# Performance work log

Measured on AMD Instinct MI355X. Metric: run time of the kernel, lower is better.

Reference implementation:

```python
import jax, jax.numpy as jnp
import numpy as np

B, T, H = 512, 512, 256
IN = 2


def setup_inputs() -> dict:
    key = jax.random.key(0)
    k1, k2, k3, k4, k5, k6 = jax.random.split(key, 6)
    inputs = jax.random.normal(k1, (B, T, IN), dtype=jnp.float32)
    # lengths in [1, T] so outputs[v-1] is always valid
    input_len = jax.random.randint(k2, (B,), 1, T + 1, dtype=jnp.int64)
    h0 = jnp.zeros((B, H), dtype=jnp.float32)
    s = 1.0 / np.sqrt(H)
    W_ih = jax.random.uniform(k3, (3 * H, IN), jnp.float32, -s, s)
    W_hh = jax.random.uniform(k4, (3 * H, H), jnp.float32, -s, s)
    b_ih = jax.random.uniform(k5, (3 * H,), jnp.float32, -s, s)
    b_hh = jax.random.uniform(k6, (3 * H,), jnp.float32, -s, s)
    return {"inputs": inputs, "input_len": input_len, "h0": h0,
            "W_ih": W_ih, "W_hh": W_hh, "b_ih": b_ih, "b_hh": b_hh}


def _gru_scan(inputs, h0, W_ih, W_hh, b_ih, b_hh):
    # Precompute input projections for all timesteps: [T, B, 3H]
    gi_all = jnp.einsum('bti,gi->tbg', inputs, W_ih) + b_ih

    def step(h, gi):
        gh = h @ W_hh.T + b_hh                      # [B, 3H]
        gi_r, gi_z, gi_n = jnp.split(gi, 3, axis=-1)
        gh_r, gh_z, gh_n = jnp.split(gh, 3, axis=-1)
        r = jax.nn.sigmoid(gi_r + gh_r)
        z = jax.nn.sigmoid(gi_z + gh_z)
        n = jnp.tanh(gi_n + r * gh_n)
        h_new = (1.0 - z) * n + z * h
        return h_new, h_new

    _, hs = jax.lax.scan(step, h0, gi_all)          # hs: [T, B, H]
    return hs


def reference(inputs, input_len, h0, W_ih, W_hh, b_ih, b_hh):
    hs = _gru_scan(inputs, h0, W_ih, W_hh, b_ih, b_hh)   # [T, B, H]
    # per-batch gather of hidden state at timestep (len - 1)
    b_idx = jnp.arange(inputs.shape[0])
    return hs[input_len - 1, b_idx]                      # [B, H]
```

## Files before the change

kernel.cpp:

```cpp
#include <hip/hip_runtime.h>
#include <stdint.h>


typedef int   v4i   __attribute__((ext_vector_type(4)));
typedef float f32x4 __attribute__((ext_vector_type(4)));

#define BB 512
#define TT 512
#define HH 256
#define NCT 48
#define KTI 4
#define HSTR8 320
#define WSCALE 2032.0f
#define INVS (1.0f/(2032.0f*127.0f))

__global__ void prep_pack_i8(const float* __restrict__ Whh, uint4* __restrict__ Wp) {
    int n = blockIdx.x * blockDim.x + threadIdx.x;
    int lane = n & 63;
    int kt = (n >> 6) & (KTI - 1);
    int ct = n >> 8;
    int row = 16 * ct + (lane & 15);
    int k0  = 64 * kt + (lane >> 4) * 16;
    const float* src = Whh + (size_t)row * HH + k0;
    uint dw[4];
    #pragma unroll
    for (int d = 0; d < 4; ++d) {
        uint acc = 0;
        #pragma unroll
        for (int j = 0; j < 4; ++j) {
            int q = (int)rintf(src[4 * d + j] * WSCALE);
            q = q < -127 ? -127 : (q > 127 ? 127 : q);
            acc |= ((uint)(q & 0xff)) << (8 * j);
        }
        dw[d] = acc;
    }
    Wp[n] = uint4{dw[0], dw[1], dw[2], dw[3]};
}

__device__ __forceinline__ float sigmoid_f(float x) {
    return __builtin_amdgcn_rcpf(1.f + __expf(-x));
}
__device__ __forceinline__ float tanh_f(float x) {
    x = fminf(fmaxf(x, -15.f), 15.f);
    float e = __expf(-2.f * x);
    return (1.f - e) * __builtin_amdgcn_rcpf(1.f + e);
}

__global__ void __launch_bounds__(512, 1)
gru_persist(const float* __restrict__ x,
            const int* __restrict__ len,
            const float* __restrict__ h0,
            const float* __restrict__ Wih,
            const float* __restrict__ bih,
            const float* __restrict__ bhh,
            const uint4* __restrict__ Wp,
            float* __restrict__ out)
{
    __shared__ __align__(16) int8_t h8[2][2][HSTR8];

    const int tid  = threadIdx.x;
    const int lane = tid & 63;
    const int w    = tid >> 6;
    const int b0   = blockIdx.x * 2;

    v4i wfr[6][KTI];
    {
        const int cts[6] = {2*w, 2*w+1, 16+2*w, 16+2*w+1, 32+2*w, 32+2*w+1};
        #pragma unroll
        for (int c = 0; c < 6; ++c)
            #pragma unroll
            for (int kt = 0; kt < KTI; ++kt)
                wfr[c][kt] = __builtin_bit_cast(v4i, Wp[(cts[c] * KTI + kt) * 64 + lane]);
    }
    #pragma unroll
    for (int c = 0; c < 6; ++c)
        #pragma unroll
        for (int kt = 0; kt < KTI; ++kt)
            asm volatile("" : "+v"(wfr[c][kt]));

    const int batch = (lane >> 4) & 1;
    const int e = 32 * w + (lane & 15) + ((lane >> 5) << 4);

    const float ccx = bih[e] + bhh[e];
    const float ccy = bih[HH + e] + bhh[HH + e];
    const float ccz = bih[2 * HH + e];
    const float ccw = bhh[2 * HH + e];
    const float wxr0 = Wih[2 * e],            wxr1 = Wih[2 * e + 1];
    const float wxz0 = Wih[2 * (HH + e)],     wxz1 = Wih[2 * (HH + e) + 1];
    const float wxn0 = Wih[2 * (2 * HH + e)], wxn1 = Wih[2 * (2 * HH + e) + 1];

    float hp = h0[(size_t)(b0 + batch) * HH + e];
    h8[0][batch][e] = (int8_t)(int)rintf(hp * 127.f);

    const int l0 = len[b0], l1 = len[b0 + 1];
    const int lm  = l0 > l1 ? l0 : l1;
    const int lmy = batch ? l1 : l0;
    const float2* xp = (const float2*)x + (size_t)(b0 + batch) * TT;
    float* op = out + (size_t)(b0 + batch) * HH + e;

    const int8_t* abase = &h8[0][(lane >> 2) & 1][(lane >> 4) * 16];

    __syncthreads();

    float2 xv = xp[0];
    #pragma unroll 1
    for (int s = 0; s < lm; ++s) {
        const float2 xvn = xp[(s + 1) & (TT - 1)];

        const float gR = fmaf(xv.x, wxr0, fmaf(xv.y, wxr1, ccx));
        const float gZ = fmaf(xv.x, wxz0, fmaf(xv.y, wxz1, ccy));
        const float gN = fmaf(xv.x, wxn0, fmaf(xv.y, wxn1, ccz));

        const int8_t* ap = abase + (s & 1) * (2 * HSTR8);
        v4i d0 = {0,0,0,0}, d1 = {0,0,0,0};
        v4i d4 = {0,0,0,0}, d5 = {0,0,0,0};
        v4i d2e = {0,0,0,0}, d2o = {0,0,0,0}, d3e = {0,0,0,0}, d3o = {0,0,0,0};

        #pragma unroll
        for (int kt = 0; kt < KTI; ++kt) {
            const v4i a = *(const v4i*)(ap + kt * 64);
            d0 = __builtin_amdgcn_mfma_i32_16x16x64_i8(a, wfr[0][kt], d0, 0, 0, 0);
            d1 = __builtin_amdgcn_mfma_i32_16x16x64_i8(a, wfr[1][kt], d1, 0, 0, 0);
            d4 = __builtin_amdgcn_mfma_i32_16x16x64_i8(a, wfr[4][kt], d4, 0, 0, 0);
            d5 = __builtin_amdgcn_mfma_i32_16x16x64_i8(a, wfr[5][kt], d5, 0, 0, 0);
        }

        const bool hi = lane >= 32;
        const float uR = (float)(hi ? d1[0] : d0[0]) * INVS;
        const float uN = (float)(hi ? d5[0] : d4[0]) * INVS;
        const float r = sigmoid_f(uR + gR);
        const float n = tanh_f(gN + r * (uN + ccw));

        #pragma unroll
        for (int kt = 0; kt < KTI; kt += 2) {
            const v4i a0 = *(const v4i*)(ap + kt * 64);
            const v4i a1 = *(const v4i*)(ap + (kt + 1) * 64);
            d2e = __builtin_amdgcn_mfma_i32_16x16x64_i8(a0, wfr[2][kt],     d2e, 0, 0, 0);
            d3e = __builtin_amdgcn_mfma_i32_16x16x64_i8(a0, wfr[3][kt],     d3e, 0, 0, 0);
            d2o = __builtin_amdgcn_mfma_i32_16x16x64_i8(a1, wfr[2][kt + 1], d2o, 0, 0, 0);
            d3o = __builtin_amdgcn_mfma_i32_16x16x64_i8(a1, wfr[3][kt + 1], d3o, 0, 0, 0);
        }

        const int uZi = hi ? (d3e[0] + d3o[0]) : (d2e[0] + d2o[0]);
        const float uZ = (float)uZi * INVS;
        const float z = sigmoid_f(uZ + gZ);
        float hn = fmaf(z, hp - n, n);
        hn = (s < lmy) ? hn : hp;
        h8[(s & 1) ^ 1][batch][e] = (int8_t)(int)rintf(hn * 127.f);
        hp = hn;
        if (s == lmy - 1) *op = hn;
        xv = xvn;
        __syncthreads();
    }
}

extern "C" void kernel_launch(void* const* d_in, const int* in_sizes, int n_in,
                              void* d_out, int out_size, void* d_ws, size_t ws_size,
                              hipStream_t stream) {
    const float* x    = (const float*)d_in[0];
    const int*   lenp = (const int*)d_in[1];
    const float* h0   = (const float*)d_in[2];
    const float* Wih  = (const float*)d_in[3];
    const float* Whh  = (const float*)d_in[4];
    const float* bih  = (const float*)d_in[5];
    const float* bhh  = (const float*)d_in[6];
    float* out = (float*)d_out;

    uint4* Wp = (uint4*)d_ws;

    prep_pack_i8<<<NCT * KTI * 64 / 256, 256, 0, stream>>>(Whh, Wp);
    gru_persist<<<BB / 2, 512, 0, stream>>>(x, lenp, h0, Wih, bih, bhh, Wp, out);
}
```

Before: 349.3 us.

## Split GRU gate columns across 16 waves instead of 8 per block

Doubles the block size to 1024 threads so each wave owns one 16-column tile per gate (R, Z, N) instead of two. This halves the per-wave MFMA chain and register-resident weights, which should shorten the serial per-timestep latency. In exchange, half of each wave's lanes are idle in the output path, and the per-step barrier must now synchronize twice as many waves.

```diff
diff --git a/kernel.cpp b/kernel.cpp
--- a/kernel.cpp
+++ b/kernel.cpp
@@ -3,7 +3,6 @@
 
 
 typedef int   v4i   __attribute__((ext_vector_type(4)));
-typedef float f32x4 __attribute__((ext_vector_type(4)));
 
 #define BB 512
 #define TT 512
@@ -46,7 +45,7 @@
     return (1.f - e) * __builtin_amdgcn_rcpf(1.f + e);
 }
 
-__global__ void __launch_bounds__(512, 1)
+__global__ void __launch_bounds__(1024, 1)
 gru_persist(const float* __restrict__ x,
             const int* __restrict__ len,
             const float* __restrict__ h0,
@@ -63,23 +62,24 @@
     const int w    = tid >> 6;
     const int b0   = blockIdx.x * 2;
 
-    v4i wfr[6][KTI];
+    v4i wfr[3][KTI];
     {
-        const int cts[6] = {2*w, 2*w+1, 16+2*w, 16+2*w+1, 32+2*w, 32+2*w+1};
+        const int cts[3] = {w, 16 + w, 32 + w};
         #pragma unroll
-        for (int c = 0; c < 6; ++c)
+        for (int c = 0; c < 3; ++c)
             #pragma unroll
             for (int kt = 0; kt < KTI; ++kt)
                 wfr[c][kt] = __builtin_bit_cast(v4i, Wp[(cts[c] * KTI + kt) * 64 + lane]);
     }
     #pragma unroll
-    for (int c = 0; c < 6; ++c)
+    for (int c = 0; c < 3; ++c)
         #pragma unroll
         for (int kt = 0; kt < KTI; ++kt)
             asm volatile("" : "+v"(wfr[c][kt]));
 
     const int batch = (lane >> 4) & 1;
-    const int e = 32 * w + (lane & 15) + ((lane >> 5) << 4);
+    const int e = 16 * w + (lane & 15);
+    const bool active = lane < 32;
 
     const float ccx = bih[e] + bhh[e];
     const float ccy = bih[HH + e] + bhh[HH + e];
@@ -90,7 +90,7 @@
     const float wxn0 = Wih[2 * (2 * HH + e)], wxn1 = Wih[2 * (2 * HH + e) + 1];
 
     float hp = h0[(size_t)(b0 + batch) * HH + e];
-    h8[0][batch][e] = (int8_t)(int)rintf(hp * 127.f);
+    if (active) h8[0][batch][e] = (int8_t)(int)rintf(hp * 127.f);
 
     const int l0 = len[b0], l1 = len[b0 + 1];
     const int lm  = l0 > l1 ? l0 : l1;
@@ -112,22 +112,18 @@
         const float gN = fmaf(xv.x, wxn0, fmaf(xv.y, wxn1, ccz));
 
         const int8_t* ap = abase + (s & 1) * (2 * HSTR8);
-        v4i d0 = {0,0,0,0}, d1 = {0,0,0,0};
-        v4i d4 = {0,0,0,0}, d5 = {0,0,0,0};
-        v4i d2e = {0,0,0,0}, d2o = {0,0,0,0}, d3e = {0,0,0,0}, d3o = {0,0,0,0};
+        v4i dR = {0,0,0,0}, dN = {0,0,0,0};
+        v4i dZe = {0,0,0,0}, dZo = {0,0,0,0};
 
         #pragma unroll
         for (int kt = 0; kt < KTI; ++kt) {
             const v4i a = *(const v4i*)(ap + kt * 64);
-            d0 = __builtin_amdgcn_mfma_i32_16x16x64_i8(a, wfr[0][kt], d0, 0, 0, 0);
-            d1 = __builtin_amdgcn_mfma_i32_16x16x64_i8(a, wfr[1][kt], d1, 0, 0, 0);
-            d4 = __builtin_amdgcn_mfma_i32_16x16x64_i8(a, wfr[4][kt], d4, 0, 0, 0);
-            d5 = __builtin_amdgcn_mfma_i32_16x16x64_i8(a, wfr[5][kt], d5, 0, 0, 0);
+            dR = __builtin_amdgcn_mfma_i32_16x16x64_i8(a, wfr[0][kt], dR, 0, 0, 0);
+            dN = __builtin_amdgcn_mfma_i32_16x16x64_i8(a, wfr[2][kt], dN, 0, 0, 0);
         }
 
-        const bool hi = lane >= 32;
-        const float uR = (float)(hi ? d1[0] : d0[0]) * INVS;
-        const float uN = (float)(hi ? d5[0] : d4[0]) * INVS;
+        const float uR = (float)dR[0] * INVS;
+        const float uN = (float)dN[0] * INVS;
         const float r = sigmoid_f(uR + gR);
         const float n = tanh_f(gN + r * (uN + ccw));
 
@@ -135,20 +131,19 @@
         for (int kt = 0; kt < KTI; kt += 2) {
             const v4i a0 = *(const v4i*)(ap + kt * 64);
             const v4i a1 = *(const v4i*)(ap + (kt + 1) * 64);
-            d2e = __builtin_amdgcn_mfma_i32_16x16x64_i8(a0, wfr[2][kt],     d2e, 0, 0, 0);
-            d3e = __builtin_amdgcn_mfma_i32_16x16x64_i8(a0, wfr[3][kt],     d3e, 0, 0, 0);
-            d2o = __builtin_amdgcn_mfma_i32_16x16x64_i8(a1, wfr[2][kt + 1], d2o, 0, 0, 0);
-            d3o = __builtin_amdgcn_mfma_i32_16x16x64_i8(a1, wfr[3][kt + 1], d3o, 0, 0, 0);
+            dZe = __builtin_amdgcn_mfma_i32_16x16x64_i8(a0, wfr[1][kt],     dZe, 0, 0, 0);
+            dZo = __builtin_amdgcn_mfma_i32_16x16x64_i8(a1, wfr[1][kt + 1], dZo, 0, 0, 0);
         }
 
-        const int uZi = hi ? (d3e[0] + d3o[0]) : (d2e[0] + d2o[0]);
-        const float uZ = (float)uZi * INVS;
+        const float uZ = (float)(dZe[0] + dZo[0]) * INVS;
         const float z = sigmoid_f(uZ + gZ);
         float hn = fmaf(z, hp - n, n);
         hn = (s < lmy) ? hn : hp;
-        h8[(s & 1) ^ 1][batch][e] = (int8_t)(int)rintf(hn * 127.f);
+        if (active) {
+            h8[(s & 1) ^ 1][batch][e] = (int8_t)(int)rintf(hn * 127.f);
+            if (s == lmy - 1) *op = hn;
+        }
         hp = hn;
-        if (s == lmy - 1) *op = hn;
         xv = xvn;
         __syncthreads();
     }
@@ -169,5 +164,5 @@
     uint4* Wp = (uint4*)d_ws;
 
     prep_pack_i8<<<NCT * KTI * 64 / 256, 256, 0, stream>>>(Whh, Wp);
-    gru_persist<<<BB / 2, 512, 0, stream>>>(x, lenp, h0, Wih, bih, bhh, Wp, out);
+    gru_persist<<<BB / 2, 1024, 0, stream>>>(x, lenp, h0, Wih, bih, bhh, Wp, out);
 }
```

Result: slower. 389.4 us (+11.5%).
